# Kernel tuning notes

Measured on AMD Instinct MI355X. Metric: run time of the kernel, lower is better.

Reference implementation:

```python
import jax, jax.numpy as jnp
import numpy as np

KH = KW = 3
STRIDE = 1
PAD = 1
DIL = 1


def setup_inputs() -> dict:
    key = jax.random.key(0)
    k1, k2, k3, k4 = jax.random.split(key, 4)
    B, C, H, W = 16, 64, 64, 64
    Cout = 64
    K = KH * KW
    x = jax.random.normal(k1, (B, C, H, W), jnp.float32)
    offset = jax.random.normal(k2, (B, 2 * K, H, W), jnp.float32)
    mask = jax.random.uniform(k3, (B, K, H, W), jnp.float32)
    # uniform(-stdv, stdv) init with stdv = 1/sqrt(C*KH*KW) ~ 0.0417; scaled normal is close enough
    weight = jax.random.normal(k4, (Cout, C, KH, KW), jnp.float32) * 0.04
    bias = jnp.zeros((Cout,), jnp.float32)  # no_bias=True -> frozen zeros, still added
    return dict(input=x, offset=offset, mask=mask, weight=weight, bias=bias)


def _bilinear(img, py, px):
    # img: [C, H, W]; py, px: [K, Ho, Wo] float sampling coords
    # DCNv2 semantics: out-of-bounds corner contributions are zero.
    H, W = img.shape[1], img.shape[2]
    y0f = jnp.floor(py)
    x0f = jnp.floor(px)
    wy = py - y0f
    wx = px - x0f
    y0 = y0f.astype(jnp.int32)
    x0 = x0f.astype(jnp.int32)
    out = jnp.zeros((img.shape[0],) + py.shape, img.dtype)
    for dy in (0, 1):
        for dx in (0, 1):
            yi = y0 + dy
            xi = x0 + dx
            valid = ((yi >= 0) & (yi < H) & (xi >= 0) & (xi < W)).astype(img.dtype)
            v = img[:, jnp.clip(yi, 0, H - 1), jnp.clip(xi, 0, W - 1)]  # [C,K,Ho,Wo]
            w = (wy if dy else 1.0 - wy) * (wx if dx else 1.0 - wx)
            out = out + v * (w * valid)[None]
    return out  # [C, K, Ho, Wo]


def reference(input, offset, mask, weight, bias):
    B, C, H, W = input.shape
    Cout, _, kh, kw = weight.shape
    K = kh * kw
    Ho = (H + 2 * PAD - (DIL * (kh - 1) + 1)) // STRIDE + 1
    Wo = (W + 2 * PAD - (DIL * (kw - 1) + 1)) // STRIDE + 1
    off = offset.reshape(B, K, 2, Ho, Wo)  # per kernel point: (dy, dx)
    ky = jnp.repeat(jnp.arange(kh), kw)  # [K] kernel row index
    kx = jnp.tile(jnp.arange(kw), kh)    # [K] kernel col index
    base_y = jnp.arange(Ho) * STRIDE - PAD
    base_x = jnp.arange(Wo) * STRIDE - PAD
    py = off[:, :, 0] + (base_y[None, None, :, None] + (ky * DIL)[None, :, None, None])
    px = off[:, :, 1] + (base_x[None, None, None, :] + (kx * DIL)[None, :, None, None])
    sampled = jax.vmap(_bilinear)(input, py, px)        # [B, C, K, Ho, Wo]
    modulated = sampled * mask[:, None]                 # mask-modulated accumulation
    out = jnp.einsum('bckpq,ock->bopq', modulated, weight.reshape(Cout, C, K))
    return out + bias[None, :, None, None]
```

## Files before the change

### kernel.cpp

```cpp
#include <hip/hip_runtime.h>

#define BATCH 16
#define C_IN  64
#define HH    64
#define WW    64
#define COUT  64
#define KK    9
#define HW    4096
#define CK    576
#define MROWB 400

typedef __bf16 bf16x8 __attribute__((ext_vector_type(8)));
typedef float  f32x16 __attribute__((ext_vector_type(16)));
typedef unsigned int u32x2 __attribute__((ext_vector_type(2)));

__device__ __forceinline__ unsigned int f32_to_bf16_rne(float f) {
    unsigned int b = __float_as_uint(f);
    b += 0x7FFFu + ((b >> 16) & 1u);
    return b >> 16;
}

__global__ __launch_bounds__(256) void prep_kernel(
    const float* __restrict__ x, const float* __restrict__ w,
    unsigned short* __restrict__ xt, unsigned short* __restrict__ wt2) {
    __shared__ unsigned short tile[64][72];
    const int t = threadIdx.x;
    const int blk = blockIdx.x;
    if (blk < 1024) {
        const int b = blk >> 6, y = blk & 63;
        const float* xrow = x + ((b * 64) * 64 + y) * 64;
#pragma unroll
        for (int it = 0; it < 4; ++it) {
            const int idx = it * 256 + t;
            const int c = idx >> 4, seg = idx & 15;
            const float4 v = *(const float4*)(xrow + c * HW + seg * 4);
            tile[seg * 4 + 0][c] = (unsigned short)f32_to_bf16_rne(v.x);
            tile[seg * 4 + 1][c] = (unsigned short)f32_to_bf16_rne(v.y);
            tile[seg * 4 + 2][c] = (unsigned short)f32_to_bf16_rne(v.z);
            tile[seg * 4 + 3][c] = (unsigned short)f32_to_bf16_rne(v.w);
        }
        __syncthreads();
#pragma unroll
        for (int it = 0; it < 2; ++it) {
            const int idx = it * 256 + t;
            const int xx = idx >> 3, cs = idx & 7;
            *(int4*)&xt[((b * HW) + y * 64 + xx) * 64 + cs * 8] =
                *(const int4*)&tile[xx][cs * 8];
        }
    } else {
        const int i = (blk - 1024) * 256 + t;
        const int j = i & 7;
        const int l = (i >> 3) & 63;
        const int ot = (i >> 9) & 1;
        const int r = i >> 10;
        const int ks = r % 12, kc = r / 12;
        const int o  = ot * 32 + (l & 31);
        const int kl = ks * 16 + (l >> 5) * 8 + j;
        const int tap = kl >> 6, c = kl & 63;
        const int k = kc * 3 + tap;
        wt2[i] = (unsigned short)f32_to_bf16_rne(w[o * CK + c * KK + k]);
    }
}

__global__ __launch_bounds__(128, 2) void dcn_main_kernel(
    const float* __restrict__ offset, const float* __restrict__ mask,
    const unsigned short* __restrict__ xt, const unsigned short* __restrict__ wt2,
    const float* __restrict__ bias, float* __restrict__ out) {
    __shared__ __align__(16) unsigned short Mlds[2][32 * (MROWB / 2)];
    __shared__ __align__(16) int PWw[2][288 * 4];
    __shared__ __align__(8) unsigned short PWa[2][288 * 4];

    const int t    = threadIdx.x;
    const int wave = __builtin_amdgcn_readfirstlane(t >> 6);
    const int lane = t & 63;
    const int quad = lane >> 4, m16 = lane & 15;
    const int n32  = lane & 31, half = lane >> 5;

    const int blk = blockIdx.x;
    const int xcd = blk & 7;
    const int i8  = blk >> 3;
    const int s   = ((i8 & 31) << 2) | (i8 >> 5);
    const int b   = (xcd << 1) | (s >> 6);
    const int row = s & 63;
    const int qb  = wave * 32;

    f32x16 acc[2];
#pragma unroll
    for (int ot = 0; ot < 2; ++ot)
#pragma unroll
        for (int r = 0; r < 16; ++r) acc[ot][r] = 0.f;

    const float* offb = offset + b * (2 * KK * HW) + row * 64;
    const float* mb   = mask + b * (KK * HW) + row * 64;
    const char* xtb   = (const char*)(xt + b * (HW * 64));
    char* MW = (char*)Mlds[wave];
    const int co = m16 * 8;

#pragma unroll
    for (int it = 0; it < 5; ++it) {
        const int item = it * 64 + lane;
        if (item < 288) {
            const int tap = item >> 5;
            const int pxi = item & 31;
            const int ky = tap / 3, kx = tap - ky * 3;
            const int q = qb + pxi;
            const float oy = __builtin_nontemporal_load(&offb[(2 * tap) * HW + q]);
            const float ox = __builtin_nontemporal_load(&offb[(2 * tap + 1) * HW + q]);
            const float mk = __builtin_nontemporal_load(&mb[tap * HW + q]);
            const float py  = oy + (float)(row - 1 + ky);
            const float pxf = ox + (float)(q - 1 + kx);
            const float y0f = floorf(py), x0f = floorf(pxf);
            const float wy = py - y0f, wx = pxf - x0f;
            const int y0 = (int)y0f, x0 = (int)x0f;
            const int y1 = y0 + 1,   x1 = x0 + 1;
            const float vy0 = (y0 >= 0 && y0 < HH) ? 1.f : 0.f;
            const float vy1 = (y1 >= 0 && y1 < HH) ? 1.f : 0.f;
            const float vx0 = (x0 >= 0 && x0 < WW) ? 1.f : 0.f;
            const float vx1 = (x1 >= 0 && x1 < WW) ? 1.f : 0.f;
            const float w00 = (1.f - wy) * (1.f - wx) * vy0 * vx0 * mk;
            const float w01 = (1.f - wy) * wx         * vy0 * vx1 * mk;
            const float w10 = wy * (1.f - wx)         * vy1 * vx0 * mk;
            const float w11 = wy * wx                 * vy1 * vx1 * mk;
            const int cy0 = min(max(y0, 0), HH - 1), cy1 = min(max(y1, 0), HH - 1);
            const int cx0 = min(max(x0, 0), WW - 1), cx1 = min(max(x1, 0), WW - 1);
            int4 P0;
            P0.x = __float_as_int(w00); P0.y = __float_as_int(w01);
            P0.z = __float_as_int(w10); P0.w = __float_as_int(w11);
            *(int4*)&PWw[wave][item * 4] = P0;
            ushort4 A;
            A.x = (unsigned short)(cy0 * 64 + cx0);
            A.y = (unsigned short)(cy0 * 64 + cx1);
            A.z = (unsigned short)(cy1 * 64 + cx0);
            A.w = (unsigned short)(cy1 * 64 + cx1);
            *(ushort4*)&PWa[wave][item * 4] = A;
        }
    }

    u32x2 g[12][4];

    auto bload = [&](int kc, int h) {
        const unsigned short* Pa = &PWa[wave][0] + (kc * 96 + h * 48) * 4;
#pragma unroll
        for (int i = 0; i < 12; ++i) {
            const int l = i * 4 + quad;
            const ushort4 a = *(const ushort4*)(Pa + l * 4);
            g[i][0] = *(const u32x2*)(xtb + ((int)a.x << 7) + co);
            g[i][1] = *(const u32x2*)(xtb + ((int)a.y << 7) + co);
            g[i][2] = *(const u32x2*)(xtb + ((int)a.z << 7) + co);
            g[i][3] = *(const u32x2*)(xtb + ((int)a.w << 7) + co);
        }
    };

    auto bfinish = [&](int kc, int h) {
        const int* Pw = &PWw[wave][0] + (kc * 96 + h * 48) * 4;
#pragma unroll
        for (int i = 0; i < 12; ++i) {
            const int l = i * 4 + quad;
            const int item = h * 48 + l;
            const int4 p0 = *(const int4*)(Pw + l * 4);
            const float fw00 = __int_as_float(p0.x), fw01 = __int_as_float(p0.y);
            const float fw10 = __int_as_float(p0.z), fw11 = __int_as_float(p0.w);
            const u32x2 u0 = g[i][0], u1 = g[i][1], u2 = g[i][2], u3 = g[i][3];
            float v0, v1, v2, v3;
            v0 = fw00 * __uint_as_float(u0.x << 16);
            v1 = fw00 * __uint_as_float(u0.x & 0xFFFF0000u);
            v2 = fw00 * __uint_as_float(u0.y << 16);
            v3 = fw00 * __uint_as_float(u0.y & 0xFFFF0000u);
            v0 = fmaf(fw01, __uint_as_float(u1.x << 16), v0);
            v1 = fmaf(fw01, __uint_as_float(u1.x & 0xFFFF0000u), v1);
            v2 = fmaf(fw01, __uint_as_float(u1.y << 16), v2);
            v3 = fmaf(fw01, __uint_as_float(u1.y & 0xFFFF0000u), v3);
            v0 = fmaf(fw10, __uint_as_float(u2.x << 16), v0);
            v1 = fmaf(fw10, __uint_as_float(u2.x & 0xFFFF0000u), v1);
            v2 = fmaf(fw10, __uint_as_float(u2.y << 16), v2);
            v3 = fmaf(fw10, __uint_as_float(u2.y & 0xFFFF0000u), v3);
            v0 = fmaf(fw11, __uint_as_float(u3.x << 16), v0);
            v1 = fmaf(fw11, __uint_as_float(u3.x & 0xFFFF0000u), v1);
            v2 = fmaf(fw11, __uint_as_float(u3.y << 16), v2);
            v3 = fmaf(fw11, __uint_as_float(u3.y & 0xFFFF0000u), v3);
            uint2 pk;
            pk.x = (f32_to_bf16_rne(v1) << 16) | f32_to_bf16_rne(v0);
            pk.y = (f32_to_bf16_rne(v3) << 16) | f32_to_bf16_rne(v2);
            *(uint2*)(MW + (item & 31) * MROWB + (item >> 5) * 128 + m16 * 8) = pk;
        }
    };

    auto phaseC = [&](int kc) {
#pragma unroll
        for (int ks = 0; ks < 12; ++ks) {
            const bf16x8 bfrag =
                *(const bf16x8*)(MW + n32 * MROWB + ks * 32 + half * 16);
#pragma unroll
            for (int ot = 0; ot < 2; ++ot) {
                const bf16x8 afrag = *(const bf16x8*)(
                    wt2 + (((kc * 12 + ks) * 2 + ot) << 9) + lane * 8);
                acc[ot] = __builtin_amdgcn_mfma_f32_32x32x16_bf16(afrag, bfrag,
                                                                  acc[ot], 0, 0, 0);
            }
        }
    };

    for (int kc = 0; kc < 3; ++kc) {
        bload(kc, 0);
        bfinish(kc, 0);
        bload(kc, 1);
        bfinish(kc, 1);
        phaseC(kc);
    }

    float* ob = out + b * (COUT * HW) + row * 64 + qb + n32;
#pragma unroll
    for (int ot = 0; ot < 2; ++ot)
#pragma unroll
        for (int r = 0; r < 16; ++r) {
            const int o = ot * 32 + (r & 3) + 8 * (r >> 2) + 4 * half;
            ob[o * HW] = acc[ot][r] + bias[o];
        }
}

extern "C" void kernel_launch(void* const* d_in, const int* in_sizes, int n_in,
                              void* d_out, int out_size, void* d_ws,
                              size_t ws_size, hipStream_t stream) {
    const float* x    = (const float*)d_in[0];
    const float* off  = (const float*)d_in[1];
    const float* mask = (const float*)d_in[2];
    const float* w    = (const float*)d_in[3];
    const float* bias = (const float*)d_in[4];
    float* out = (float*)d_out;

    unsigned short* xt  = (unsigned short*)d_ws;
    unsigned short* wt2 = (unsigned short*)((char*)d_ws + 8388608);

    prep_kernel<<<1024 + 144, 256, 0, stream>>>(x, w, xt, wt2);
    dcn_main_kernel<<<1024, 128, 0, stream>>>(off, mask, xt, wt2, bias, out);
}
```

Measured before the change: 113.7 us.

## Split input channels across two blocks with atomic accumulation into bias-initialized output

The main kernel is split along input channels into two halves. The grid grows to 2048 blocks, each gathering only 32 channels and running half the MFMA K-steps, with results combined through atomicAdd into an output that the prep kernel pre-fills with bias. The weight packing and the LDS row stride are reorganized to match, and the bilinear gather is restructured so each lane handles an 8-channel slice. This is meant to raise parallelism and occupancy, at the cost of recomputing offsets and bilinear weights in both halves, extra output writes and atomic traffic, and a non-deterministic summation order.

New measurement: 126.0 us. +10.8%, slower.

```diff
diff --git a/kernel.cpp b/kernel.cpp
--- a/kernel.cpp
+++ b/kernel.cpp
@@ -8,7 +8,7 @@
 #define KK    9
 #define HW    4096
 #define CK    576
-#define MROWB 400
+#define MROWB 208
 
 typedef __bf16 bf16x8 __attribute__((ext_vector_type(8)));
 typedef float  f32x16 __attribute__((ext_vector_type(16)));
@@ -19,14 +19,21 @@
     b += 0x7FFFu + ((b >> 16) & 1u);
     return b >> 16;
 }
+__device__ __forceinline__ float bf16lo(unsigned int u) {
+    return __uint_as_float(u << 16);
+}
+__device__ __forceinline__ float bf16hi(unsigned int u) {
+    return __uint_as_float(u & 0xFFFF0000u);
+}
 
 __global__ __launch_bounds__(256) void prep_kernel(
     const float* __restrict__ x, const float* __restrict__ w,
-    unsigned short* __restrict__ xt, unsigned short* __restrict__ wt2) {
-    __shared__ unsigned short tile[64][72];
+    const float* __restrict__ bias, unsigned short* __restrict__ xt,
+    unsigned short* __restrict__ wt2, float* __restrict__ out) {
     const int t = threadIdx.x;
     const int blk = blockIdx.x;
     if (blk < 1024) {
+        __shared__ unsigned short tile[64][72];
         const int b = blk >> 6, y = blk & 63;
         const float* xrow = x + ((b * 64) * 64 + y) * 64;
 #pragma unroll
@@ -47,25 +54,33 @@
             *(int4*)&xt[((b * HW) + y * 64 + xx) * 64 + cs * 8] =
                 *(const int4*)&tile[xx][cs * 8];
         }
-    } else {
+    } else if (blk < 1312) {
         const int i = (blk - 1024) * 256 + t;
         const int j = i & 7;
         const int l = (i >> 3) & 63;
         const int ot = (i >> 9) & 1;
         const int r = i >> 10;
-        const int ks = r % 12, kc = r / 12;
+        const int ks = r % 6, kc = (r / 6) % 3, h2 = r / 18;
         const int o  = ot * 32 + (l & 31);
         const int kl = ks * 16 + (l >> 5) * 8 + j;
-        const int tap = kl >> 6, c = kl & 63;
-        const int k = kc * 3 + tap;
-        wt2[i] = (unsigned short)f32_to_bf16_rne(w[o * CK + c * KK + k]);
+        const int tap = kl >> 5, c = h2 * 32 + (kl & 31);
+        wt2[i] = (unsigned short)f32_to_bf16_rne(w[o * CK + c * KK + kc * 3 + tap]);
+    } else {
+        const int blkz = blk - 1312;
+#pragma unroll
+        for (int it = 0; it < 4; ++it) {
+            const int idx = blkz * 4096 + it * 1024 + t * 4;
+            const float bv = bias[(idx >> 12) & 63];
+            float4 v; v.x = bv; v.y = bv; v.z = bv; v.w = bv;
+            *(float4*)(out + idx) = v;
+        }
     }
 }
 
 __global__ __launch_bounds__(128, 2) void dcn_main_kernel(
     const float* __restrict__ offset, const float* __restrict__ mask,
     const unsigned short* __restrict__ xt, const unsigned short* __restrict__ wt2,
-    const float* __restrict__ bias, float* __restrict__ out) {
+    float* __restrict__ out) {
     __shared__ __align__(16) unsigned short Mlds[2][32 * (MROWB / 2)];
     __shared__ __align__(16) int PWw[2][288 * 4];
     __shared__ __align__(8) unsigned short PWa[2][288 * 4];
@@ -73,13 +88,15 @@
     const int t    = threadIdx.x;
     const int wave = __builtin_amdgcn_readfirstlane(t >> 6);
     const int lane = t & 63;
-    const int quad = lane >> 4, m16 = lane & 15;
-    const int n32  = lane & 31, half = lane >> 5;
+    const int oct  = lane >> 3, octl = lane & 7;
+    const int n32  = lane & 31, h16 = lane >> 5;
 
     const int blk = blockIdx.x;
     const int xcd = blk & 7;
     const int i8  = blk >> 3;
-    const int s   = ((i8 & 31) << 2) | (i8 >> 5);
+    const int h2  = i8 & 1;
+    const int s7  = i8 >> 1;
+    const int s   = ((s7 & 15) << 3) | (s7 >> 4);
     const int b   = (xcd << 1) | (s >> 6);
     const int row = s & 63;
     const int qb  = wave * 32;
@@ -92,21 +109,19 @@
 
     const float* offb = offset + b * (2 * KK * HW) + row * 64;
     const float* mb   = mask + b * (KK * HW) + row * 64;
-    const char* xtb   = (const char*)(xt + b * (HW * 64));
+    const char* xtbh  = (const char*)(xt + b * (HW * 64)) + h2 * 64 + octl * 8;
     char* MW = (char*)Mlds[wave];
-    const int co = m16 * 8;
 
 #pragma unroll
     for (int it = 0; it < 5; ++it) {
         const int item = it * 64 + lane;
         if (item < 288) {
-            const int tap = item >> 5;
-            const int pxi = item & 31;
+            const int tap = item >> 5, pxi = item & 31;
             const int ky = tap / 3, kx = tap - ky * 3;
             const int q = qb + pxi;
-            const float oy = __builtin_nontemporal_load(&offb[(2 * tap) * HW + q]);
-            const float ox = __builtin_nontemporal_load(&offb[(2 * tap + 1) * HW + q]);
-            const float mk = __builtin_nontemporal_load(&mb[tap * HW + q]);
+            const float oy = offb[(2 * tap) * HW + q];
+            const float ox = offb[(2 * tap + 1) * HW + q];
+            const float mk = mb[tap * HW + q];
             const float py  = oy + (float)(row - 1 + ky);
             const float pxf = ox + (float)(q - 1 + kx);
             const float y0f = floorf(py), x0f = floorf(pxf);
@@ -136,76 +151,53 @@
         }
     }
 
+    ushort4 a[12];
     u32x2 g[12][4];
 
-    auto bload = [&](int kc, int h) {
-        const unsigned short* Pa = &PWa[wave][0] + (kc * 96 + h * 48) * 4;
-#pragma unroll
-        for (int i = 0; i < 12; ++i) {
-            const int l = i * 4 + quad;
-            const ushort4 a = *(const ushort4*)(Pa + l * 4);
-            g[i][0] = *(const u32x2*)(xtb + ((int)a.x << 7) + co);
-            g[i][1] = *(const u32x2*)(xtb + ((int)a.y << 7) + co);
-            g[i][2] = *(const u32x2*)(xtb + ((int)a.z << 7) + co);
-            g[i][3] = *(const u32x2*)(xtb + ((int)a.w << 7) + co);
-        }
-    };
-
-    auto bfinish = [&](int kc, int h) {
-        const int* Pw = &PWw[wave][0] + (kc * 96 + h * 48) * 4;
-#pragma unroll
-        for (int i = 0; i < 12; ++i) {
-            const int l = i * 4 + quad;
-            const int item = h * 48 + l;
-            const int4 p0 = *(const int4*)(Pw + l * 4);
-            const float fw00 = __int_as_float(p0.x), fw01 = __int_as_float(p0.y);
-            const float fw10 = __int_as_float(p0.z), fw11 = __int_as_float(p0.w);
-            const u32x2 u0 = g[i][0], u1 = g[i][1], u2 = g[i][2], u3 = g[i][3];
+    for (int kc = 0; kc < 3; ++kc) {
+#pragma unroll
+        for (int grp = 0; grp < 12; ++grp)
+            a[grp] = *(const ushort4*)&PWa[wave][(kc * 96 + grp * 8 + oct) * 4];
+#pragma unroll
+        for (int grp = 0; grp < 12; ++grp) {
+            g[grp][0] = *(const u32x2*)(xtbh + ((int)a[grp].x << 7));
+            g[grp][1] = *(const u32x2*)(xtbh + ((int)a[grp].y << 7));
+            g[grp][2] = *(const u32x2*)(xtbh + ((int)a[grp].z << 7));
+            g[grp][3] = *(const u32x2*)(xtbh + ((int)a[grp].w << 7));
+        }
+#pragma unroll
+        for (int grp = 0; grp < 12; ++grp) {
+            const int ic = grp * 8 + oct;
+            const float4 w4 = *(const float4*)&PWw[wave][(kc * 96 + ic) * 4];
+            const u32x2 u0 = g[grp][0], u1 = g[grp][1];
+            const u32x2 u2 = g[grp][2], u3 = g[grp][3];
             float v0, v1, v2, v3;
-            v0 = fw00 * __uint_as_float(u0.x << 16);
-            v1 = fw00 * __uint_as_float(u0.x & 0xFFFF0000u);
-            v2 = fw00 * __uint_as_float(u0.y << 16);
-            v3 = fw00 * __uint_as_float(u0.y & 0xFFFF0000u);
-            v0 = fmaf(fw01, __uint_as_float(u1.x << 16), v0);
-            v1 = fmaf(fw01, __uint_as_float(u1.x & 0xFFFF0000u), v1);
-            v2 = fmaf(fw01, __uint_as_float(u1.y << 16), v2);
-            v3 = fmaf(fw01, __uint_as_float(u1.y & 0xFFFF0000u), v3);
-            v0 = fmaf(fw10, __uint_as_float(u2.x << 16), v0);
-            v1 = fmaf(fw10, __uint_as_float(u2.x & 0xFFFF0000u), v1);
-            v2 = fmaf(fw10, __uint_as_float(u2.y << 16), v2);
-            v3 = fmaf(fw10, __uint_as_float(u2.y & 0xFFFF0000u), v3);
-            v0 = fmaf(fw11, __uint_as_float(u3.x << 16), v0);
-            v1 = fmaf(fw11, __uint_as_float(u3.x & 0xFFFF0000u), v1);
-            v2 = fmaf(fw11, __uint_as_float(u3.y << 16), v2);
-            v3 = fmaf(fw11, __uint_as_float(u3.y & 0xFFFF0000u), v3);
+            v0 = w4.x * bf16lo(u0.x);  v1 = w4.x * bf16hi(u0.x);
+            v2 = w4.x * bf16lo(u0.y);  v3 = w4.x * bf16hi(u0.y);
+            v0 = fmaf(w4.y, bf16lo(u1.x), v0);  v1 = fmaf(w4.y, bf16hi(u1.x), v1);
+            v2 = fmaf(w4.y, bf16lo(u1.y), v2);  v3 = fmaf(w4.y, bf16hi(u1.y), v3);
+            v0 = fmaf(w4.z, bf16lo(u2.x), v0);  v1 = fmaf(w4.z, bf16hi(u2.x), v1);
+            v2 = fmaf(w4.z, bf16lo(u2.y), v2);  v3 = fmaf(w4.z, bf16hi(u2.y), v3);
+            v0 = fmaf(w4.w, bf16lo(u3.x), v0);  v1 = fmaf(w4.w, bf16hi(u3.x), v1);
+            v2 = fmaf(w4.w, bf16lo(u3.y), v2);  v3 = fmaf(w4.w, bf16hi(u3.y), v3);
             uint2 pk;
             pk.x = (f32_to_bf16_rne(v1) << 16) | f32_to_bf16_rne(v0);
             pk.y = (f32_to_bf16_rne(v3) << 16) | f32_to_bf16_rne(v2);
-            *(uint2*)(MW + (item & 31) * MROWB + (item >> 5) * 128 + m16 * 8) = pk;
-        }
-    };
-
-    auto phaseC = [&](int kc) {
-#pragma unroll
-        for (int ks = 0; ks < 12; ++ks) {
+            const int tap = ic >> 5, pxi = ic & 31;
+            *(uint2*)(MW + pxi * MROWB + tap * 64 + octl * 8) = pk;
+        }
+#pragma unroll
+        for (int ks = 0; ks < 6; ++ks) {
             const bf16x8 bfrag =
-                *(const bf16x8*)(MW + n32 * MROWB + ks * 32 + half * 16);
+                *(const bf16x8*)(MW + n32 * MROWB + ks * 32 + h16 * 16);
 #pragma unroll
             for (int ot = 0; ot < 2; ++ot) {
                 const bf16x8 afrag = *(const bf16x8*)(
-                    wt2 + (((kc * 12 + ks) * 2 + ot) << 9) + lane * 8);
+                    wt2 + (((((h2 * 3 + kc) * 6 + ks) << 1) + ot) << 9) + lane * 8);
                 acc[ot] = __builtin_amdgcn_mfma_f32_32x32x16_bf16(afrag, bfrag,
                                                                   acc[ot], 0, 0, 0);
             }
         }
-    };
-
-    for (int kc = 0; kc < 3; ++kc) {
-        bload(kc, 0);
-        bfinish(kc, 0);
-        bload(kc, 1);
-        bfinish(kc, 1);
-        phaseC(kc);
     }
 
     float* ob = out + b * (COUT * HW) + row * 64 + qb + n32;
@@ -213,8 +205,8 @@
     for (int ot = 0; ot < 2; ++ot)
 #pragma unroll
         for (int r = 0; r < 16; ++r) {
-            const int o = ot * 32 + (r & 3) + 8 * (r >> 2) + 4 * half;
-            ob[o * HW] = acc[ot][r] + bias[o];
+            const int o = ot * 32 + (r & 3) + 8 * (r >> 2) + 4 * h16;
+            atomicAdd(&ob[o * HW], acc[ot][r]);
         }
 }
 
@@ -231,6 +223,6 @@
     unsigned short* xt  = (unsigned short*)d_ws;
     unsigned short* wt2 = (unsigned short*)((char*)d_ws + 8388608);
 
-    prep_kernel<<<1024 + 144, 256, 0, stream>>>(x, w, xt, wt2);
-    dcn_main_kernel<<<1024, 128, 0, stream>>>(off, mask, xt, wt2, bias, out);
-}
+    prep_kernel<<<1024 + 288 + 1024, 256, 0, stream>>>(x, w, bias, xt, wt2, out);
+    dcn_main_kernel<<<2048, 128, 0, stream>>>(off, mask, xt, wt2, out);
+}
```
